# Kernel optimization log

Measured on AMD Instinct MI355X. Metric: run time of the kernel, lower is better.

Reference implementation:

```python
import jax, jax.numpy as jnp
import numpy as np

B, S, DIM = 2, 2048, 1024
N_HEAD, HEAD_DIM = 16, 64


def setup_inputs() -> dict:
    key = jax.random.key(0)
    k1, k2, k3, k4 = jax.random.split(key, 4)
    x = jax.random.normal(k1, (B, S, DIM), dtype=jnp.float32)
    # rotary table: cos/sin pairs, shape [S, head_dim//2, 2]
    half = HEAD_DIM // 2
    inv_freq = 1.0 / (10000.0 ** (jnp.arange(0, half, dtype=jnp.float32) / half))
    t = jnp.arange(S, dtype=jnp.float32)
    ang = t[:, None] * inv_freq[None, :]
    freqs_cis = jnp.stack([jnp.cos(ang), jnp.sin(ang)], axis=-1)  # [S, half, 2]
    # causal boolean mask [1,1,S,S] (True = attend)
    mask = jnp.tril(jnp.ones((S, S), dtype=bool))[None, None]
    wqkv = jax.random.normal(k2, (3 * DIM, DIM), dtype=jnp.float32) * (DIM ** -0.5)
    wo = jax.random.normal(k3, (DIM, DIM), dtype=jnp.float32) * (DIM ** -0.5)
    return {"x": x, "freqs_cis": freqs_cis, "mask": mask, "wqkv": wqkv, "wo": wo}


def apply_rotary_emb(x, freqs_cis):
    # x: [B, S, H, D]; freqs_cis: [S, D//2, 2]
    xs = x.reshape(*x.shape[:-1], -1, 2)  # [B,S,H,D//2,2]
    fc = freqs_cis[None, :, None, :, :]  # [1,S,1,D//2,2]
    xr, xi = xs[..., 0], xs[..., 1]
    cr, ci = fc[..., 0], fc[..., 1]
    out = jnp.stack([xr * cr - xi * ci, xi * cr + xr * ci], axis=-1)
    return out.reshape(x.shape)


def reference(x, freqs_cis, mask, wqkv, wo):
    bsz, seqlen, _ = x.shape
    qkv = jnp.einsum('bsd,ed->bse', x, wqkv)  # [B,S,3*dim]
    q, k, v = jnp.split(qkv, 3, axis=-1)
    q = q.reshape(bsz, seqlen, N_HEAD, HEAD_DIM)
    k = k.reshape(bsz, seqlen, N_HEAD, HEAD_DIM)
    v = v.reshape(bsz, seqlen, N_HEAD, HEAD_DIM)
    q = apply_rotary_emb(q, freqs_cis)
    k = apply_rotary_emb(k, freqs_cis)
    scale = HEAD_DIM ** -0.5
    scores = jnp.einsum('bqhd,bkhd->bhqk', q, k) * scale  # [B,H,S,S]
    scores = jnp.where(mask, scores, jnp.finfo(scores.dtype).min)
    attn = jax.nn.softmax(scores, axis=-1)
    y = jnp.einsum('bhqk,bkhd->bqhd', attn, v).reshape(bsz, seqlen, N_HEAD * HEAD_DIM)
    return jnp.einsum('bse,de->bsd', y, wo)
```

## Files before the change

### kernel.cpp

```cpp
#include <hip/hip_runtime.h>
#include <hip/hip_bf16.h>
#include <stdint.h>


typedef __attribute__((ext_vector_type(8))) __bf16 bf16x8;
typedef __attribute__((ext_vector_type(4))) float f32x4;

union B8 { uint4 u; bf16x8 v; unsigned short us[8]; };

static __device__ __forceinline__ unsigned short f2bf(float f) {
  union { float f; unsigned int ui; } x; x.f = f;
  unsigned int r = x.ui + 0x7fffu + ((x.ui >> 16) & 1u);
  return (unsigned short)(r >> 16);
}
static __device__ __forceinline__ f32x4 mfma16(bf16x8 a, bf16x8 b, f32x4 c) {
  return __builtin_amdgcn_mfma_f32_16x16x32_bf16(a, b, c, 0, 0, 0);
}
#define AS1 __attribute__((address_space(1)))
#define AS3 __attribute__((address_space(3)))
static __device__ __forceinline__ void gload_lds16(const void* g, void* l) {
  __builtin_amdgcn_global_load_lds((const AS1 unsigned int*)g,
                                   (AS3 unsigned int*)l, 16, 0, 0);
}

__global__ __launch_bounds__(256) void cvt_kernel(
    const float* __restrict__ src, unsigned short* __restrict__ dst, int n4) {
  int i = blockIdx.x * 256 + threadIdx.x;
  if (i < n4) {
    float4 f = ((const float4*)src)[i];
    ushort4 u;
    u.x = f2bf(f.x); u.y = f2bf(f.y); u.z = f2bf(f.z); u.w = f2bf(f.w);
    ((ushort4*)dst)[i] = u;
  }
}

__global__ __launch_bounds__(256) void qkv_rope_kernel(
    const unsigned short* __restrict__ xb,
    const unsigned short* __restrict__ wqkvb,
    const float* __restrict__ freqs,
    unsigned short* __restrict__ Q,
    unsigned short* __restrict__ K,
    unsigned short* __restrict__ Vt)
{
  __shared__ __align__(16) unsigned short As[128 * 64];
  __shared__ __align__(16) unsigned short Bs[128 * 64];
  const int t = threadIdx.x;
  const int lane = t & 63, wv = t >> 6;
  const int c = lane & 15, quad = lane >> 4;
  const int wm = wv >> 1, wn = wv & 1;
  const int tm = blockIdx.x & 31, tn = blockIdx.x >> 5;
  const int m0 = tm * 128, n0 = tn * 128;

  f32x4 acc[4][4] = {};

  for (int k0 = 0; k0 < 1024; k0 += 64) {
    for (int r = 0; r < 4; ++r) {
      int cid = t + 256 * r;
      int row = cid >> 3, jc = cid & 7;
      int sc = jc ^ (row & 7);
      gload_lds16(xb    + (size_t)(m0 + row) * 1024 + k0 + sc * 8, (char*)As + cid * 16);
      gload_lds16(wqkvb + (size_t)(n0 + row) * 1024 + k0 + sc * 8, (char*)Bs + cid * 16);
    }
    __syncthreads();
    for (int ks = 0; ks < 2; ++ks) {
      bf16x8 a[4], b[4];
      for (int st = 0; st < 4; ++st) {
        int ra = wm * 64 + st * 16 + c;
        int sa = (ks * 4 + quad) ^ (ra & 7);
        a[st] = *(const bf16x8*)((const char*)As + ra * 128 + sa * 16);
        int rb = wn * 64 + st * 16 + c;
        int sb = (ks * 4 + quad) ^ (rb & 7);
        b[st] = *(const bf16x8*)((const char*)Bs + rb * 128 + sb * 16);
      }
      for (int sm = 0; sm < 4; ++sm)
        for (int sn = 0; sn < 4; ++sn)
          acc[sm][sn] = mfma16(a[sm], b[sn], acc[sm][sn]);
    }
    __syncthreads();
  }

  for (int sm = 0; sm < 4; ++sm) {
    for (int sn = 0; sn < 4; ++sn) {
      const int e = n0 + wn * 64 + sn * 16 + c;
      const int seg = e >> 10;
      const int eh = e & 1023;
      const int h = eh >> 6, d = eh & 63;
      for (int i = 0; i < 4; ++i) {
        const int m = m0 + wm * 64 + sm * 16 + quad * 4 + i;
        const int b_ = m >> 11, s_ = m & 2047;
        float v = acc[sm][sn][i];
        if (seg == 2) {
          Vt[((size_t)(b_ * 16 + h) * 64 + d) * 2048 + s_] = f2bf(v);
        } else {
          float partner = __shfl_xor(v, 1, 64);
          const int p = d >> 1;
          float cr = freqs[s_ * 64 + p * 2];
          float ci = freqs[s_ * 64 + p * 2 + 1];
          float outv = (d & 1) ? (v * cr + partner * ci) : (v * cr - partner * ci);
          unsigned short* dst = (seg == 0) ? Q : K;
          dst[((size_t)(b_ * 16 + h) * 2048 + s_) * 64 + d] = f2bf(outv);
        }
      }
    }
  }
}

struct QState {
  bf16x8 qf0, qf1;
  f32x4 o[4];
  float lp[4];
};

static __device__ __forceinline__ void attn_chunk(
    QState& st, const char* Ks, const char* Vs, float* myp,
    int c, int quad, int k0, int q0, bool diag)
{
  f32x4 sfr[4];
  for (int kc = 0; kc < 4; ++kc) {
    const int key = kc * 16 + c;
    const int s0 = quad ^ (key & 7), s1 = (4 + quad) ^ (key & 7);
    f32x4 sacc = {};
    sacc = mfma16(st.qf0, *(const bf16x8*)(Ks + key * 128 + s0 * 16), sacc);
    sacc = mfma16(st.qf1, *(const bf16x8*)(Ks + key * 128 + s1 * 16), sacc);
    sfr[kc] = sacc;
  }
  for (int i = 0; i < 4; ++i) {
    const int qrow = q0 + quad * 4 + i;
    float e[4];
    for (int kc = 0; kc < 4; ++kc) {
      float arg = fmaf(sfr[kc][i], 0.18033688f, -20.19773057f);
      if (diag && (k0 + kc * 16 + c > qrow)) arg = -1e30f;
      e[kc] = exp2f(arg);
    }
    st.lp[i] += (e[0] + e[1]) + (e[2] + e[3]);
    const int prow = (quad * 4 + i) * 68;
    myp[prow + c]      = e[0];
    myp[prow + 16 + c] = e[1];
    myp[prow + 32 + c] = e[2];
    myp[prow + 48 + c] = e[3];
  }
  bf16x8 pf[2];
  for (int sH = 0; sH < 2; ++sH) {
    const float* src = myp + c * 68 + sH * 32 + quad * 8;
    float4 f0 = *(const float4*)(src);
    float4 f1 = *(const float4*)(src + 4);
    B8 p;
    p.us[0] = f2bf(f0.x); p.us[1] = f2bf(f0.y);
    p.us[2] = f2bf(f0.z); p.us[3] = f2bf(f0.w);
    p.us[4] = f2bf(f1.x); p.us[5] = f2bf(f1.y);
    p.us[6] = f2bf(f1.z); p.us[7] = f2bf(f1.w);
    pf[sH] = p.v;
  }
  for (int ct = 0; ct < 4; ++ct) {
    const int d = ct * 16 + c;
    const int s0 = quad ^ (d & 7), s1 = (4 + quad) ^ (d & 7);
    st.o[ct] = mfma16(pf[0], *(const bf16x8*)(Vs + d * 128 + s0 * 16), st.o[ct]);
    st.o[ct] = mfma16(pf[1], *(const bf16x8*)(Vs + d * 128 + s1 * 16), st.o[ct]);
  }
}

__global__ __launch_bounds__(256) void attn_kernel(
    const unsigned short* __restrict__ Q,
    const unsigned short* __restrict__ K,
    const unsigned short* __restrict__ Vt,
    unsigned short* __restrict__ Y)
{
  __shared__ __align__(16) unsigned short Ks[64 * 64];
  __shared__ __align__(16) unsigned short Vs[64 * 64];
  __shared__ __align__(16) float plds[4][16 * 68];
  const int t = threadIdx.x;
  const int lane = t & 63, wv = t >> 6;
  const int c = lane & 15, quad = lane >> 4;
  const int j = blockIdx.x >> 5, bh = blockIdx.x & 31;
  const int b = bh >> 4, h = bh & 15;
  const int qA = j * 64 + wv * 16;
  const int qB = (31 - j) * 64 + wv * 16;

  const unsigned short* Qb = Q + (size_t)bh * (2048 * 64);
  const unsigned short* Kb = K + (size_t)bh * (2048 * 64);
  const unsigned short* Vb = Vt + (size_t)bh * (64 * 2048);

  QState A = {}, Bst = {};
  A.qf0 = *(const bf16x8*)(Qb + (qA + c) * 64 + quad * 8);
  A.qf1 = *(const bf16x8*)(Qb + (qA + c) * 64 + 32 + quad * 8);
  Bst.qf0 = *(const bf16x8*)(Qb + (qB + c) * 64 + quad * 8);
  Bst.qf1 = *(const bf16x8*)(Qb + (qB + c) * 64 + 32 + quad * 8);

  const int nkt = 32 - j;
  float* myp = plds[wv];

  for (int kt = 0; kt < nkt; ++kt) {
    const int k0 = kt * 64;
    __syncthreads();
    for (int r = 0; r < 2; ++r) {
      int cid = t + 256 * r;
      int row = cid >> 3, jc = cid & 7;
      int sc = jc ^ (row & 7);
      gload_lds16(Kb + (size_t)(k0 + row) * 64 + sc * 8, (char*)Ks + cid * 16);
      gload_lds16(Vb + (size_t)row * 2048 + k0 + sc * 8, (char*)Vs + cid * 16);
    }
    __syncthreads();

    attn_chunk(Bst, (const char*)Ks, (const char*)Vs, myp, c, quad,
               k0, qB, kt == 31 - j);
    if (kt <= j)
      attn_chunk(A, (const char*)Ks, (const char*)Vs, myp, c, quad,
                 k0, qA, kt == j);
  }

  for (int set = 0; set < 2; ++set) {
    QState& st = set ? Bst : A;
    const int q0 = set ? qB : qA;
    for (int i = 0; i < 4; ++i) {
      float l = st.lp[i];
      l += __shfl_xor(l, 1, 16);
      l += __shfl_xor(l, 2, 16);
      l += __shfl_xor(l, 4, 16);
      l += __shfl_xor(l, 8, 16);
      float inv = 1.0f / l;
      const int s = q0 + quad * 4 + i;
      unsigned short* dst = Y + ((size_t)(b * 2048 + s)) * 1024 + h * 64;
      for (int ct = 0; ct < 4; ++ct)
        dst[ct * 16 + c] = f2bf(st.o[ct][i] * inv);
    }
  }
}

__global__ __launch_bounds__(256) void out_proj_kernel(
    const unsigned short* __restrict__ Y,
    const unsigned short* __restrict__ wob,
    float* __restrict__ out)
{
  __shared__ __align__(16) unsigned short As[128 * 64];
  __shared__ __align__(16) unsigned short Bs[128 * 64];
  const int t = threadIdx.x;
  const int lane = t & 63, wv = t >> 6;
  const int c = lane & 15, quad = lane >> 4;
  const int wm = wv >> 1, wn = wv & 1;
  const int tm = blockIdx.x & 31, tn = blockIdx.x >> 5;
  const int m0 = tm * 128, n0 = tn * 128;

  f32x4 acc[4][4] = {};

  for (int k0 = 0; k0 < 1024; k0 += 64) {
    for (int r = 0; r < 4; ++r) {
      int cid = t + 256 * r;
      int row = cid >> 3, jc = cid & 7;
      int sc = jc ^ (row & 7);
      gload_lds16(Y   + (size_t)(m0 + row) * 1024 + k0 + sc * 8, (char*)As + cid * 16);
      gload_lds16(wob + (size_t)(n0 + row) * 1024 + k0 + sc * 8, (char*)Bs + cid * 16);
    }
    __syncthreads();
    for (int ks = 0; ks < 2; ++ks) {
      bf16x8 a[4], b[4];
      for (int st = 0; st < 4; ++st) {
        int ra = wm * 64 + st * 16 + c;
        int sa = (ks * 4 + quad) ^ (ra & 7);
        a[st] = *(const bf16x8*)((const char*)As + ra * 128 + sa * 16);
        int rb = wn * 64 + st * 16 + c;
        int sb = (ks * 4 + quad) ^ (rb & 7);
        b[st] = *(const bf16x8*)((const char*)Bs + rb * 128 + sb * 16);
      }
      for (int sm = 0; sm < 4; ++sm)
        for (int sn = 0; sn < 4; ++sn)
          acc[sm][sn] = mfma16(a[sm], b[sn], acc[sm][sn]);
    }
    __syncthreads();
  }

  for (int sm = 0; sm < 4; ++sm)
    for (int sn = 0; sn < 4; ++sn)
      for (int i = 0; i < 4; ++i) {
        const int m = m0 + wm * 64 + sm * 16 + quad * 4 + i;
        const int e = n0 + wn * 64 + sn * 16 + c;
        out[(size_t)m * 1024 + e] = acc[sm][sn][i];
      }
}

extern "C" void kernel_launch(void* const* d_in, const int* in_sizes, int n_in,
                              void* d_out, int out_size, void* d_ws, size_t ws_size,
                              hipStream_t stream) {
  const float* x     = (const float*)d_in[0];
  const float* freqs = (const float*)d_in[1];
  const float* wqkv  = (const float*)d_in[3];
  const float* wo    = (const float*)d_in[4];
  float* out = (float*)d_out;

  const size_t BHSD = (size_t)2 * 16 * 2048 * 64;
  unsigned short* Q     = (unsigned short*)d_ws;
  unsigned short* K     = Q + BHSD;
  unsigned short* Vt    = K + BHSD;
  unsigned short* Y     = Vt + BHSD;
  unsigned short* xb    = Y + BHSD;
  unsigned short* wqkvb = xb + 4194304;
  unsigned short* wob   = wqkvb + 3145728;

  cvt_kernel<<<4096, 256, 0, stream>>>(x,    xb,    4194304 / 4);
  cvt_kernel<<<3072, 256, 0, stream>>>(wqkv, wqkvb, 3145728 / 4);
  cvt_kernel<<<1024, 256, 0, stream>>>(wo,   wob,   1048576 / 4);
  qkv_rope_kernel<<<768, 256, 0, stream>>>(xb, wqkvb, freqs, Q, K, Vt);
  attn_kernel<<<512, 256, 0, stream>>>(Q, K, Vt, Y);
  out_proj_kernel<<<256, 256, 0, stream>>>(Y, wob, out);
}
```

Measured before the change: 233.4 us.

## Split attention KV range across two blocks, merge convert launches, shrink out-proj tiles

```diff
diff --git a/kernel.cpp b/kernel.cpp
--- a/kernel.cpp
+++ b/kernel.cpp
@@ -8,6 +8,9 @@
 
 union B8 { uint4 u; bf16x8 v; unsigned short us[8]; };
 
+static __device__ __forceinline__ float bf2f(unsigned short u) {
+  union { unsigned int ui; float f; } x; x.ui = ((unsigned int)u) << 16; return x.f;
+}
 static __device__ __forceinline__ unsigned short f2bf(float f) {
   union { float f; unsigned int ui; } x; x.f = f;
   unsigned int r = x.ui + 0x7fffu + ((x.ui >> 16) & 1u);
@@ -23,15 +26,20 @@
                                    (AS3 unsigned int*)l, 16, 0, 0);
 }
 
-__global__ __launch_bounds__(256) void cvt_kernel(
-    const float* __restrict__ src, unsigned short* __restrict__ dst, int n4) {
+__global__ __launch_bounds__(256) void cvt_all_kernel(
+    const float* __restrict__ x, const float* __restrict__ wqkv,
+    const float* __restrict__ wo,
+    unsigned short* __restrict__ xb, unsigned short* __restrict__ wqkvb,
+    unsigned short* __restrict__ wob) {
   int i = blockIdx.x * 256 + threadIdx.x;
-  if (i < n4) {
-    float4 f = ((const float4*)src)[i];
-    ushort4 u;
-    u.x = f2bf(f.x); u.y = f2bf(f.y); u.z = f2bf(f.z); u.w = f2bf(f.w);
-    ((ushort4*)dst)[i] = u;
-  }
+  const float* src; unsigned short* dst; int off;
+  if (i < 1048576)       { src = x;    dst = xb;    off = i; }
+  else if (i < 1835008)  { src = wqkv; dst = wqkvb; off = i - 1048576; }
+  else                   { src = wo;   dst = wob;   off = i - 1835008; }
+  float4 f = ((const float4*)src)[off];
+  ushort4 u;
+  u.x = f2bf(f.x); u.y = f2bf(f.y); u.z = f2bf(f.z); u.w = f2bf(f.w);
+  ((ushort4*)dst)[off] = u;
 }
 
 __global__ __launch_bounds__(256) void qkv_rope_kernel(
@@ -159,6 +167,95 @@
   }
 }
 
+__global__ __launch_bounds__(256, 4) void attn_partial_kernel(
+    const unsigned short* __restrict__ Q,
+    const unsigned short* __restrict__ K,
+    const unsigned short* __restrict__ Vt,
+    unsigned short* __restrict__ Po,
+    float* __restrict__ Pl)
+{
+  __shared__ __align__(16) unsigned short Ks[64 * 64];
+  __shared__ __align__(16) unsigned short Vs[64 * 64];
+  __shared__ __align__(16) float plds[4][16 * 68];
+  const int t = threadIdx.x;
+  const int lane = t & 63, wv = t >> 6;
+  const int c = lane & 15, quad = lane >> 4;
+  const int bh = blockIdx.x & 31;
+  const int rest = blockIdx.x >> 5;
+  const int j = rest >> 1, half = rest & 1;
+  const int qA = j * 64 + wv * 16;
+  const int qB = (31 - j) * 64 + wv * 16;
+
+  const unsigned short* Qb = Q + (size_t)bh * (2048 * 64);
+  const unsigned short* Kb = K + (size_t)bh * (2048 * 64);
+  const unsigned short* Vb = Vt + (size_t)bh * (64 * 2048);
+
+  QState A = {}, Bst = {};
+  A.qf0 = *(const bf16x8*)(Qb + (qA + c) * 64 + quad * 8);
+  A.qf1 = *(const bf16x8*)(Qb + (qA + c) * 64 + 32 + quad * 8);
+  Bst.qf0 = *(const bf16x8*)(Qb + (qB + c) * 64 + quad * 8);
+  Bst.qf1 = *(const bf16x8*)(Qb + (qB + c) * 64 + 32 + quad * 8);
+
+  float* myp = plds[wv];
+  const int ktmax = 31 - j;
+
+  for (int kt = half; kt <= ktmax; kt += 2) {
+    const int k0 = kt * 64;
+    __syncthreads();
+    for (int r = 0; r < 2; ++r) {
+      int cid = t + 256 * r;
+      int row = cid >> 3, jc = cid & 7;
+      int sc = jc ^ (row & 7);
+      gload_lds16(Kb + (size_t)(k0 + row) * 64 + sc * 8, (char*)Ks + cid * 16);
+      gload_lds16(Vb + (size_t)row * 2048 + k0 + sc * 8, (char*)Vs + cid * 16);
+    }
+    __syncthreads();
+    attn_chunk(Bst, (const char*)Ks, (const char*)Vs, myp, c, quad,
+               k0, qB, kt == ktmax);
+    if (kt <= j)
+      attn_chunk(A, (const char*)Ks, (const char*)Vs, myp, c, quad,
+                 k0, qA, kt == j);
+  }
+
+  unsigned short* Poh = Po + (size_t)half * (32 * 2048 * 64) + (size_t)bh * (2048 * 64);
+  float* Plh = Pl + (size_t)half * (32 * 2048) + bh * 2048;
+  for (int set = 0; set < 2; ++set) {
+    QState& st = set ? Bst : A;
+    const int q0 = set ? qB : qA;
+    for (int i = 0; i < 4; ++i) {
+      float l = st.lp[i];
+      l += __shfl_xor(l, 1, 16);
+      l += __shfl_xor(l, 2, 16);
+      l += __shfl_xor(l, 4, 16);
+      l += __shfl_xor(l, 8, 16);
+      const int s = q0 + quad * 4 + i;
+      for (int ct = 0; ct < 4; ++ct)
+        Poh[(size_t)s * 64 + ct * 16 + c] = f2bf(st.o[ct][i]);
+      if (c == 0) Plh[s] = l;
+    }
+  }
+}
+
+__global__ __launch_bounds__(256) void combine_kernel(
+    const unsigned short* __restrict__ Po, const float* __restrict__ Pl,
+    unsigned short* __restrict__ Yb)
+{
+  const int idx = blockIdx.x * 256 + threadIdx.x;
+  const int bh = idx >> 14, rem = idx & 16383;
+  const int s = rem >> 3, g = rem & 7;
+  const size_t base = (size_t)bh * (2048 * 64) + (size_t)s * 64 + g * 8;
+  B8 a, b;
+  a.u = *(const uint4*)(Po + base);
+  b.u = *(const uint4*)(Po + (size_t)(32 * 2048 * 64) + base);
+  float l = Pl[bh * 2048 + s] + Pl[32 * 2048 + bh * 2048 + s];
+  float inv = 1.0f / l;
+  B8 y;
+  for (int k = 0; k < 8; ++k)
+    y.us[k] = f2bf((bf2f(a.us[k]) + bf2f(b.us[k])) * inv);
+  const int b_ = bh >> 4, h = bh & 15;
+  *(uint4*)(Yb + ((size_t)(b_ * 2048 + s)) * 1024 + h * 64 + g * 8) = y.u;
+}
+
 __global__ __launch_bounds__(256) void attn_kernel(
     const unsigned short* __restrict__ Q,
     const unsigned short* __restrict__ K,
@@ -200,7 +297,6 @@
       gload_lds16(Vb + (size_t)row * 2048 + k0 + sc * 8, (char*)Vs + cid * 16);
     }
     __syncthreads();
-
     attn_chunk(Bst, (const char*)Ks, (const char*)Vs, myp, c, quad,
                k0, qB, kt == 31 - j);
     if (kt <= j)
@@ -231,19 +327,19 @@
     const unsigned short* __restrict__ wob,
     float* __restrict__ out)
 {
-  __shared__ __align__(16) unsigned short As[128 * 64];
-  __shared__ __align__(16) unsigned short Bs[128 * 64];
+  __shared__ __align__(16) unsigned short As[64 * 64];
+  __shared__ __align__(16) unsigned short Bs[64 * 64];
   const int t = threadIdx.x;
   const int lane = t & 63, wv = t >> 6;
   const int c = lane & 15, quad = lane >> 4;
   const int wm = wv >> 1, wn = wv & 1;
-  const int tm = blockIdx.x & 31, tn = blockIdx.x >> 5;
-  const int m0 = tm * 128, n0 = tn * 128;
-
-  f32x4 acc[4][4] = {};
+  const int tm = blockIdx.x & 63, tn = blockIdx.x >> 6;
+  const int m0 = tm * 64, n0 = tn * 64;
+
+  f32x4 acc[2][2] = {};
 
   for (int k0 = 0; k0 < 1024; k0 += 64) {
-    for (int r = 0; r < 4; ++r) {
+    for (int r = 0; r < 2; ++r) {
       int cid = t + 256 * r;
       int row = cid >> 3, jc = cid & 7;
       int sc = jc ^ (row & 7);
@@ -252,27 +348,27 @@
     }
     __syncthreads();
     for (int ks = 0; ks < 2; ++ks) {
-      bf16x8 a[4], b[4];
-      for (int st = 0; st < 4; ++st) {
-        int ra = wm * 64 + st * 16 + c;
+      bf16x8 a[2], b[2];
+      for (int st = 0; st < 2; ++st) {
+        int ra = wm * 32 + st * 16 + c;
         int sa = (ks * 4 + quad) ^ (ra & 7);
         a[st] = *(const bf16x8*)((const char*)As + ra * 128 + sa * 16);
-        int rb = wn * 64 + st * 16 + c;
+        int rb = wn * 32 + st * 16 + c;
         int sb = (ks * 4 + quad) ^ (rb & 7);
         b[st] = *(const bf16x8*)((const char*)Bs + rb * 128 + sb * 16);
       }
-      for (int sm = 0; sm < 4; ++sm)
-        for (int sn = 0; sn < 4; ++sn)
+      for (int sm = 0; sm < 2; ++sm)
+        for (int sn = 0; sn < 2; ++sn)
           acc[sm][sn] = mfma16(a[sm], b[sn], acc[sm][sn]);
     }
     __syncthreads();
   }
 
-  for (int sm = 0; sm < 4; ++sm)
-    for (int sn = 0; sn < 4; ++sn)
+  for (int sm = 0; sm < 2; ++sm)
+    for (int sn = 0; sn < 2; ++sn)
       for (int i = 0; i < 4; ++i) {
-        const int m = m0 + wm * 64 + sm * 16 + quad * 4 + i;
-        const int e = n0 + wn * 64 + sn * 16 + c;
+        const int m = m0 + wm * 32 + sm * 16 + quad * 4 + i;
+        const int e = n0 + wn * 32 + sn * 16 + c;
         out[(size_t)m * 1024 + e] = acc[sm][sn][i];
       }
 }
@@ -290,15 +386,23 @@
   unsigned short* Q     = (unsigned short*)d_ws;
   unsigned short* K     = Q + BHSD;
   unsigned short* Vt    = K + BHSD;
-  unsigned short* Y     = Vt + BHSD;
-  unsigned short* xb    = Y + BHSD;
+  unsigned short* Yb    = Vt + BHSD;
+  unsigned short* xb    = Yb + BHSD;
   unsigned short* wqkvb = xb + 4194304;
   unsigned short* wob   = wqkvb + 3145728;
-
-  cvt_kernel<<<4096, 256, 0, stream>>>(x,    xb,    4194304 / 4);
-  cvt_kernel<<<3072, 256, 0, stream>>>(wqkv, wqkvb, 3145728 / 4);
-  cvt_kernel<<<1024, 256, 0, stream>>>(wo,   wob,   1048576 / 4);
+  unsigned short* Po    = wob + 1048576;
+  float*          Pl    = (float*)(Po + 2 * BHSD);
+
+  const size_t need_fast =
+      (size_t)((char*)(Pl + 2 * 32 * 2048) - (char*)d_ws);
+
+  cvt_all_kernel<<<8192, 256, 0, stream>>>(x, wqkv, wo, xb, wqkvb, wob);
   qkv_rope_kernel<<<768, 256, 0, stream>>>(xb, wqkvb, freqs, Q, K, Vt);
-  attn_kernel<<<512, 256, 0, stream>>>(Q, K, Vt, Y);
-  out_proj_kernel<<<256, 256, 0, stream>>>(Y, wob, out);
-}
+  if (ws_size >= need_fast) {
+    attn_partial_kernel<<<1024, 256, 0, stream>>>(Q, K, Vt, Po, Pl);
+    combine_kernel<<<2048, 256, 0, stream>>>(Po, Pl, Yb);
+  } else {
+    attn_kernel<<<512, 256, 0, stream>>>(Q, K, Vt, Yb);
+  }
+  out_proj_kernel<<<1024, 256, 0, stream>>>(Yb, wob, out);
+}
```

Measured after the change: 295.4 us. +26.6%, slower.
